# Optimization experiments

Measured on AMD Instinct MI355X. Metric: run time of the kernel, lower is better.

Reference implementation:

```python
import jax, jax.numpy as jnp
import numpy as np

L_LAYERS = 2
SEQ = 2048
K_EIG = 24
D = 128
D_TGT = 64
K_U = 3
K_Y = 2
B = 8


def hankel_eigh(n, k):
    # Z[i,j] = 2 / ((i+j)^3 - (i+j)), 1-indexed; top-k eigenpairs
    s = np.arange(1, n + 1, dtype=np.float64)
    ij = s[:, None] + s[None, :]
    z = 2.0 / (ij ** 3 - ij)
    vals, vecs = np.linalg.eigh(z)
    return (jnp.asarray(vals[-k:], jnp.float32), jnp.asarray(vecs[:, -k:], jnp.float32))


def setup_inputs() -> dict:
    key = jax.random.key(0)
    ks = jax.random.split(key, 8)
    sd = 1.0 / np.sqrt(D)
    inp = {
        "x": jax.random.normal(ks[0], (B, SEQ, D), jnp.float32),
        "emb_w": jax.random.normal(ks[1], (D, D), jnp.float32) * sd,
        "emb_b": jnp.zeros((D,), jnp.float32),
        "ln_g": jnp.ones((L_LAYERS, D), jnp.float32),
        "ln_b": jnp.zeros((L_LAYERS, D), jnp.float32),
        "m_phi": jax.random.normal(ks[2], (L_LAYERS, K_EIG * D, D), jnp.float32) * sd,
        "m_u": jax.random.normal(ks[3], (L_LAYERS, D, D, K_U), jnp.float32) * sd,
        "m_y": jax.random.normal(ks[4], (L_LAYERS, D, K_Y, D), jnp.float32) * 0.01,
        "w1": jax.random.normal(ks[5], (L_LAYERS, D, 2 * D), jnp.float32) * sd,
        "b1": jnp.zeros((L_LAYERS, 2 * D), jnp.float32),
        "proj_w": jax.random.normal(ks[6], (D, D_TGT), jnp.float32) * sd,
        "proj_b": jnp.zeros((D_TGT,), jnp.float32),
    }
    ev, evec = hankel_eigh(SEQ, K_EIG)
    inp["eig_vals"] = ev
    inp["eig_vecs"] = evec
    return inp


def compute_x_tilde(x, eig_vals, eig_vecs):
    # x: [B, L, D]; causal (truncated full) convolution of each eigvec filter
    # with each input channel via FFT. Result [B, L, K, D] -> [B, L, K*D].
    n = 2 * SEQ
    V = jnp.fft.rfft(eig_vecs, n=n, axis=0)              # [nf, K]
    U = jnp.fft.rfft(x, n=n, axis=1)                     # [B, nf, D]
    conv = jnp.fft.irfft(V[None, :, :, None] * U[:, :, None, :], n=n, axis=1)[:, :SEQ]
    conv = conv * (eig_vals ** 0.25)[None, None, :, None]
    return conv.reshape(x.shape[0], SEQ, K_EIG * x.shape[-1]).astype(x.dtype)


def compute_ar_x_preds(m_u, x):
    # o[t] = sum_{i<K_U} m_u[:, :, i] @ x[t-i]  (zero for t-i < 0)
    res = jnp.einsum('bli,oi->blo', x, m_u[:, :, 0])
    for i in range(1, K_U):
        xi = jnp.pad(x, ((0, 0), (i, 0), (0, 0)))[:, :SEQ]
        res = res + jnp.einsum('bli,oi->blo', xi, m_u[:, :, i])
    return res


def compute_y_t(m_y, deltas):
    # y[t] = sum_{j<K_Y} m_y[:, j, :] @ y[t-1-j] + deltas[t]
    d = deltas.shape[-1]
    def step(carry, x):  # carry [B, K_Y, d] holds y[t-1], y[t-2], ...
        out = jnp.einsum('okd,bkd->bo', m_y, carry) + x
        carry = jnp.concatenate([out[:, None, :], carry[:, :-1]], axis=1)
        return carry, out
    init = jnp.zeros((deltas.shape[0], K_Y, d), deltas.dtype)
    _, ys = jax.lax.scan(step, init, jnp.swapaxes(deltas, 0, 1))
    return jnp.swapaxes(ys, 0, 1)


def layer_norm(x, g, b):
    mu = x.mean(-1, keepdims=True)
    var = ((x - mu) ** 2).mean(-1, keepdims=True)
    return (x - mu) / jnp.sqrt(var + 1e-5) * g + b


def reference(x, emb_w, emb_b, ln_g, ln_b, m_phi, m_u, m_y, w1, b1, proj_w, proj_b, eig_vals, eig_vecs):
    h = x @ emb_w + emb_b
    for i in range(L_LAYERS):
        z = h
        h = layer_norm(h, ln_g[i], ln_b[i])
        x_tilde = compute_x_tilde(h, eig_vals, eig_vecs)       # [B, L, K*D]
        delta = x_tilde @ m_phi[i] + compute_ar_x_preds(m_u[i], h)
        y = compute_y_t(m_y[i], delta)
        y = jax.nn.gelu(y, approximate=False)
        y = y @ w1[i] + b1[i]
        a, g = jnp.split(y, 2, axis=-1)
        h = a * jax.nn.sigmoid(g) + z                          # GLU + residual (dropout=0)
    return h @ proj_w + proj_b
```

## Files before the change

### kernel.cpp

```cpp
#include <hip/hip_runtime.h>

typedef unsigned short u16;
typedef unsigned int u32;
typedef __bf16 bf16x8 __attribute__((ext_vector_type(8)));
typedef float f32x4 __attribute__((ext_vector_type(4)));
typedef float f32x2 __attribute__((ext_vector_type(2)));
typedef u16 u16x4 __attribute__((ext_vector_type(4)));
typedef u16 u16x8 __attribute__((ext_vector_type(8)));

#define DEV static __device__ __forceinline__

static constexpr int ROWS = 8 * 2048;
static constexpr int TAPS = 24;
static constexpr int PADR = 64;
static constexpr int DROWS = 2048 + PADR;

DEV u16 f2bf(float x) {
  u32 u = __float_as_uint(x);
  u += 0x7fffu + ((u >> 16) & 1u);
  return (u16)(u >> 16);
}

DEV void gld_lds16(const u16* g, u16* l) {
  __builtin_amdgcn_global_load_lds(
      (const __attribute__((address_space(1))) u32*)g,
      (__attribute__((address_space(3))) u32*)l, 16, 0, 0);
}


__global__ void prep_toeplitz(const float* __restrict__ evec,
                              const float* __restrict__ evals,
                              u16* __restrict__ T) {
  int k = blockIdx.x / 33, ti = blockIdx.x % 33;
  float sc = powf(evals[k], 0.25f);
  u16* out = T + (size_t)blockIdx.x * 4096;
  for (int e = threadIdx.x; e < 4096; e += 256) {
    int i = e >> 6, j = e & 63;
    int tau = (ti - 1) * 64 + i - j;
    float v = (tau >= 0 && tau < 2048) ? evec[tau * 24 + k] * sc : 0.f;
    out[e] = f2bf(v);
  }
}

__global__ __launch_bounds__(128) void hprep_kernel(const float* __restrict__ my,
                                                    u16* __restrict__ Hp) {
  const int l = blockIdx.x >> 7, j = blockIdx.x & 127;
  const int o = threadIdx.x;
  const float* M = my + (size_t)l * 32768;
  u32 mp1[64], mp2[64];
  {
    const float* r1 = M + (size_t)o * 256;
    const float* r2 = r1 + 128;
#pragma unroll
    for (int q = 0; q < 64; ++q) {
      mp1[q] = (u32)f2bf(r1[2 * q]) | ((u32)f2bf(r1[2 * q + 1]) << 16);
      mp2[q] = (u32)f2bf(r2[2 * q]) | ((u32)f2bf(r2[2 * q + 1]) << 16);
    }
  }
  __shared__ float vb[3][128];
  u16* HpL = Hp + ((size_t)l * 128 + o) * (TAPS * 128) + j;
  float v0 = (o == j) ? 1.f : 0.f;
  vb[0][o] = v0;
  vb[2][o] = 0.f;
  HpL[0] = f2bf(v0);
  __syncthreads();
  for (int tau = 1; tau < TAPS; ++tau) {
    const int a = (tau + 2) % 3;
    const int b = (tau + 1) % 3;
    const int c = tau % 3;
    const float* v1 = vb[a];
    const float* v2 = vb[b];
    float acc = 0.f;
#pragma unroll
    for (int q = 0; q < 64; ++q) {
      u32 w1 = mp1[q], w2 = mp2[q];
      float m1lo = __uint_as_float(w1 << 16);
      float m1hi = __uint_as_float(w1 & 0xffff0000u);
      float m2lo = __uint_as_float(w2 << 16);
      float m2hi = __uint_as_float(w2 & 0xffff0000u);
      acc += m1lo * v1[2 * q] + m1hi * v1[2 * q + 1];
      acc += m2lo * v2[2 * q] + m2hi * v2[2 * q + 1];
    }
    vb[c][o] = acc;
    HpL[tau * 128] = f2bf(acc);
    __syncthreads();
  }
}

__global__ __launch_bounds__(256) void prep_misc(
    const float* __restrict__ emb_w, const float* __restrict__ w1,
    const float* __restrict__ proj_w, const float* __restrict__ mphi,
    const float* __restrict__ mu, const float* __restrict__ x,
    u16* __restrict__ embT, u16* __restrict__ w1T, u16* __restrict__ projT,
    u16* __restrict__ mphiT, u16* __restrict__ xbf, u16* __restrict__ dpad,
    u16* __restrict__ xtc) {
  const int blk = blockIdx.x, tid = threadIdx.x;
  if (blk < 64) {
    int idx = blk * 256 + tid;
    int n = idx >> 7, k = idx & 127;
    embT[idx] = f2bf(emb_w[k * 128 + n]);
  } else if (blk < 320) {
    int l = (blk - 64) >> 7;
    int idx = ((blk - 64) & 127) * 256 + tid;
    int n = idx >> 7, k = idx & 127;
    w1T[l * 32768 + idx] = f2bf(w1[l * 32768 + k * 256 + n]);
  } else if (blk < 352) {
    int idx = (blk - 320) * 256 + tid;
    int n = idx >> 7, k = idx & 127;
    projT[idx] = f2bf(proj_w[k * 64 + n]);
  } else if (blk < 3808) {
    int l = (blk - 352) / 1728;
    int idx = ((blk - 352) % 1728) * 256 + tid;
    int o = idx / 3456, c = idx % 3456;
    float v;
    if (c < 3072) {
      v = mphi[(size_t)l * 3072 * 128 + (size_t)c * 128 + o];
    } else {
      int cc = c - 3072;
      int j = cc >> 7, i = cc & 127;
      v = mu[(size_t)l * 128 * 128 * 3 + ((size_t)o * 128 + i) * 3 + j];
    }
    mphiT[(size_t)l * 128 * 3456 + idx] = f2bf(v);
  } else if (blk < 5856) {
    int i = (blk - 3808) * 256 + tid;
    f32x4 v = *(const f32x4*)(x + (size_t)i * 4);
    u16x4 o;
    o[0] = f2bf(v[0]); o[1] = f2bf(v[1]); o[2] = f2bf(v[2]); o[3] = f2bf(v[3]);
    *(u16x4*)(xbf + (size_t)i * 4) = o;
  } else if (blk < 5888) {
    int i = (blk - 5856) * 256 + tid;
    int b = i >> 10, off = i & 1023;
    *(u16x8*)(dpad + (size_t)b * DROWS * 128 + off * 8) =
        (u16x8){0, 0, 0, 0, 0, 0, 0, 0};
  } else {
    for (int e = tid; e < 3072; e += 256) {
      int b = e / 384, r = e % 384;
      size_t addr;
      if (r < 256) addr = ((size_t)b * 2048 + 0) * 3456 + 3200 + r;
      else addr = ((size_t)b * 2048 + 1) * 3456 + 3328 + (r - 256);
      xtc[addr] = 0;
    }
  }
}


__global__ __launch_bounds__(256) void ln_tr_kernel(
    const float* __restrict__ h, const float* __restrict__ gam,
    const float* __restrict__ bet, u16* __restrict__ hlnT,
    u16* __restrict__ xtc) {
  __shared__ u16 tile[64][136];
  const int b = blockIdx.x >> 5, st = blockIdx.x & 31;
  const int wrow = threadIdx.x >> 6;
  const int lane = threadIdx.x & 63;
  f32x2 g2 = *(const f32x2*)(gam + lane * 2);
  f32x2 b2 = *(const f32x2*)(bet + lane * 2);
#pragma unroll 4
  for (int it = 0; it < 16; ++it) {
    int lr = it * 4 + wrow;
    int t = st * 64 + lr;
    size_t row = (size_t)b * 2048 + t;
    f32x2 v = *(const f32x2*)(h + row * 128 + lane * 2);
    float s = v[0] + v[1];
#pragma unroll
    for (int o = 32; o; o >>= 1) s += __shfl_xor(s, o);
    float mu = s * (1.f / 128.f);
    float dx = v[0] - mu, dy = v[1] - mu;
    float q = dx * dx + dy * dy;
#pragma unroll
    for (int o = 32; o; o >>= 1) q += __shfl_xor(q, o);
    float rstd = rsqrtf(q * (1.f / 128.f) + 1e-5f);
    float o0 = dx * rstd * g2[0] + b2[0];
    float o1 = dy * rstd * g2[1] + b2[1];
    u32 pk = (u32)f2bf(o0) | ((u32)f2bf(o1) << 16);
    *(u32*)&tile[lr][lane * 2] = pk;
    *(u32*)&xtc[row * 3456 + 3072 + lane * 2] = pk;
    if (t + 1 < 2048) *(u32*)&xtc[(row + 1) * 3456 + 3200 + lane * 2] = pk;
    if (t + 2 < 2048) *(u32*)&xtc[(row + 2) * 3456 + 3328 + lane * 2] = pk;
  }
  __syncthreads();
  const int d = threadIdx.x >> 1;
  const int half = threadIdx.x & 1;
#pragma unroll
  for (int i = 0; i < 4; ++i) {
    int sg = half * 4 + i;
    u16x8 w;
#pragma unroll
    for (int j = 0; j < 8; ++j) w[j] = tile[sg * 8 + j][d];
    *(u16x8*)(hlnT + ((size_t)b * 128 + d) * 2048 + st * 64 + sg * 8) = w;
  }
}


template <int BM, int BN, int WROWS, int WCOLS>
__global__ __launch_bounds__(256) void gemm_bt(
    const u16* __restrict__ A, int lda, const u16* __restrict__ BT, int ldbt,
    float* __restrict__ C, int ldc, const float* __restrict__ bias, int kBlocks) {
  constexpr int WTM = BM / WROWS;
  constexpr int WTN = BN / WCOLS;
  constexpr int FM = WTM / 16;
  constexpr int FN = WTN / 16;
  static_assert(FM >= 1 && FN >= 1, "tile too small");
  __shared__ u16 As[BM * 64];
  __shared__ u16 Bs[BN * 64];
  const int tid = threadIdx.x;
  const int wid = tid >> 6, lane = tid & 63;
  const int bm = blockIdx.x, bn = blockIdx.y;
  const int wr = wid / WCOLS, wc = wid % WCOLS;
  const int r = lane & 15, hi = lane >> 4;

  f32x4 acc[FM][FN];
#pragma unroll
  for (int i = 0; i < FM; ++i)
#pragma unroll
    for (int j = 0; j < FN; ++j) acc[i][j] = (f32x4){0.f, 0.f, 0.f, 0.f};

  for (int kb = 0; kb < kBlocks; ++kb) {
    if (kb) __syncthreads();
#pragma unroll
    for (int it = 0; it < BM / 32; ++it) {
      int ci = it * 256 + tid;
      int sc = (ci & 7) ^ ((ci >> 3) & 7);
      gld_lds16(A + (size_t)(bm * BM + (ci >> 3)) * lda + kb * 64 + sc * 8,
                &As[(it * 256 + wid * 64) * 8]);
    }
#pragma unroll
    for (int it = 0; it < BN / 32; ++it) {
      int ci = it * 256 + tid;
      int sc = (ci & 7) ^ ((ci >> 3) & 7);
      gld_lds16(BT + (size_t)(bn * BN + (ci >> 3)) * ldbt + kb * 64 + sc * 8,
                &Bs[(it * 256 + wid * 64) * 8]);
    }
    __syncthreads();
#pragma unroll
    for (int ks = 0; ks < 2; ++ks) {
      const int sk = ((ks * 4 + hi) ^ (r & 7)) << 3;
      bf16x8 af[FM], bfv[FN];
#pragma unroll
      for (int fm = 0; fm < FM; ++fm)
        af[fm] = *(const bf16x8*)&As[(wr * WTM + fm * 16 + r) * 64 + sk];
#pragma unroll
      for (int fn = 0; fn < FN; ++fn)
        bfv[fn] = *(const bf16x8*)&Bs[(wc * WTN + fn * 16 + r) * 64 + sk];
#pragma unroll
      for (int fm = 0; fm < FM; ++fm)
#pragma unroll
        for (int fn = 0; fn < FN; ++fn)
          acc[fm][fn] = __builtin_amdgcn_mfma_f32_16x16x32_bf16(
              af[fm], bfv[fn], acc[fm][fn], 0, 0, 0);
    }
  }
#pragma unroll
  for (int fm = 0; fm < FM; ++fm) {
#pragma unroll
    for (int fn = 0; fn < FN; ++fn) {
      const int col = bn * BN + wc * WTN + fn * 16 + r;
      const float bv = bias ? bias[col] : 0.f;
#pragma unroll
      for (int q = 0; q < 4; ++q) {
        const int row = bm * BM + wr * WTM + fm * 16 + hi * 4 + q;
        C[(size_t)row * ldc + col] = acc[fm][fn][q] + bv;
      }
    }
  }
}

__global__ __launch_bounds__(256) void gemm_delta(
    const u16* __restrict__ A, const u16* __restrict__ BT,
    u16* __restrict__ dpad) {
  __shared__ u16 As[2][32 * 64];
  __shared__ u16 Bs[2][128 * 64];
  const int tid = threadIdx.x;
  const int wid = tid >> 6, lane = tid & 63;
  const int bm = blockIdx.x;
  const int wr = wid >> 1, wc = wid & 1;
  const int r = lane & 15, hi = lane >> 4;

  f32x4 acc[4];
#pragma unroll
  for (int j = 0; j < 4; ++j) acc[j] = (f32x4){0.f, 0.f, 0.f, 0.f};

  auto stage = [&](int kb, int p) {
    {
      int ci = tid;
      int sc = (ci & 7) ^ ((ci >> 3) & 7);
      gld_lds16(A + (size_t)(bm * 32 + (ci >> 3)) * 3456 + kb * 64 + sc * 8,
                &As[p][(wid * 64) * 8]);
    }
#pragma unroll
    for (int it = 0; it < 4; ++it) {
      int ci = it * 256 + tid;
      int sc = (ci & 7) ^ ((ci >> 3) & 7);
      gld_lds16(BT + (size_t)(ci >> 3) * 3456 + kb * 64 + sc * 8,
                &Bs[p][(it * 256 + wid * 64) * 8]);
    }
  };

  stage(0, 0);
  __syncthreads();
  for (int kb = 0; kb < 54; ++kb) {
    const int p = kb & 1;
    if (kb < 53) stage(kb + 1, p ^ 1);
#pragma unroll
    for (int ks = 0; ks < 2; ++ks) {
      const int sk = ((ks * 4 + hi) ^ (r & 7)) << 3;
      bf16x8 af = *(const bf16x8*)&As[p][(wr * 16 + r) * 64 + sk];
      bf16x8 bfv[4];
#pragma unroll
      for (int fn = 0; fn < 4; ++fn)
        bfv[fn] = *(const bf16x8*)&Bs[p][(wc * 64 + fn * 16 + r) * 64 + sk];
#pragma unroll
      for (int fn = 0; fn < 4; ++fn)
        acc[fn] = __builtin_amdgcn_mfma_f32_16x16x32_bf16(af, bfv[fn], acc[fn], 0, 0, 0);
    }
    __syncthreads();
  }
#pragma unroll
  for (int fn = 0; fn < 4; ++fn) {
    const int col = wc * 64 + fn * 16 + r;
#pragma unroll
    for (int q = 0; q < 4; ++q) {
      const int row = bm * 32 + wr * 16 + hi * 4 + q;
      int bb = row >> 11, t = row & 2047;
      dpad[((size_t)(bb * DROWS + PADR + t)) * 128 + col] = f2bf(acc[fn][q]);
    }
  }
}

__global__ __launch_bounds__(256) void gemm_conv(
    const u16* __restrict__ T, const u16* __restrict__ hlnT,
    u16* __restrict__ xtc) {
  __shared__ u16 As[2][64 * 64];
  __shared__ u16 Bs[128 * 64];
  const int tid = threadIdx.x;
  const int wid = tid >> 6, lane = tid & 63;
  const int xcd = blockIdx.x & 7;
  const int slot = blockIdx.x >> 3;
  const int tt = slot / 24;
  const int rem24 = slot % 24;
  const int kc = (xcd >> 1) * 6 + rem24 % 6;
  const int b = (xcd & 1) * 4 + rem24 / 6;
  const int t0 = (15 - tt) << 7;
  const int r = lane & 15, hi = lane >> 4;
  const int wr = wid >> 1, wc = wid & 1;

  f32x4 acc[4][4];
#pragma unroll
  for (int i = 0; i < 4; ++i)
#pragma unroll
    for (int j = 0; j < 4; ++j) acc[i][j] = (f32x4){0.f, 0.f, 0.f, 0.f};

  const u16* Tk = T + (size_t)kc * 33 * 4096;
  const u16* Bb = hlnT + (size_t)b * 128 * 2048;
  const int base = t0 >> 6;
  const int nsb = base + 2;

  for (int sb = 0; sb < nsb; ++sb) {
    const int dlt = base - sb;
    const int p = sb & 1;
    if (sb) __syncthreads();
#pragma unroll
    for (int it = 0; it < 2; ++it) {
      int ci = it * 256 + tid;
      int sc = (ci & 7) ^ ((ci >> 3) & 7);
      gld_lds16(Tk + (size_t)(dlt + 1) * 4096 + (ci >> 3) * 64 + sc * 8,
                &As[p][(it * 256 + wid * 64) * 8]);
    }
    if (sb == 0) {
#pragma unroll
      for (int it = 0; it < 2; ++it) {
        int ci = it * 256 + tid;
        int sc = (ci & 7) ^ ((ci >> 3) & 7);
        gld_lds16(Tk + (size_t)(dlt + 2) * 4096 + (ci >> 3) * 64 + sc * 8,
                  &As[1][(it * 256 + wid * 64) * 8]);
      }
    }
#pragma unroll
    for (int it = 0; it < 4; ++it) {
      int ci = it * 256 + tid;
      int sc = (ci & 7) ^ ((ci >> 3) & 7);
      gld_lds16(Bb + (size_t)(ci >> 3) * 2048 + sb * 64 + sc * 8,
                &Bs[(it * 256 + wid * 64) * 8]);
    }
    __syncthreads();
    const u16* Aw = As[p ^ wr];
#pragma unroll
    for (int ks = 0; ks < 2; ++ks) {
      const int sk = ((ks * 4 + hi) ^ (r & 7)) << 3;
      bf16x8 af[4], bfv[4];
#pragma unroll
      for (int fm = 0; fm < 4; ++fm)
        af[fm] = *(const bf16x8*)&Aw[(fm * 16 + r) * 64 + sk];
#pragma unroll
      for (int fn = 0; fn < 4; ++fn)
        bfv[fn] = *(const bf16x8*)&Bs[(wc * 64 + fn * 16 + r) * 64 + sk];
#pragma unroll
      for (int fm = 0; fm < 4; ++fm)
#pragma unroll
        for (int fn = 0; fn < 4; ++fn)
          acc[fm][fn] = __builtin_amdgcn_mfma_f32_16x16x32_bf16(
              af[fm], bfv[fn], acc[fm][fn], 0, 0, 0);
    }
  }
#pragma unroll
  for (int fm = 0; fm < 4; ++fm) {
#pragma unroll
    for (int fn = 0; fn < 4; ++fn) {
      const int col = wc * 64 + fn * 16 + r;
#pragma unroll
      for (int q = 0; q < 4; ++q) {
        const int row = t0 + wr * 64 + fm * 16 + hi * 4 + q;
        xtc[((size_t)(b * 2048 + row)) * 3456 + kc * 128 + col] = f2bf(acc[fm][fn][q]);
      }
    }
  }
}

__global__ __launch_bounds__(256) void gemm_yconv(
    const u16* __restrict__ dpad, const u16* __restrict__ Hp,
    u16* __restrict__ ybf) {
  __shared__ u16 As[64 * 128];
  __shared__ u16 Bs[64 * 128];
  const int tid = threadIdx.x;
  const int wid = tid >> 6, lane = tid & 63;
  const int bm = blockIdx.x, bn = blockIdx.y;
  const int b = bm >> 5, t0 = (bm & 31) << 6;
  const int r = lane & 15, hi = lane >> 4;

  f32x4 acc[4];
#pragma unroll
  for (int j = 0; j < 4; ++j) acc[j] = (f32x4){0.f, 0.f, 0.f, 0.f};

  const u16* Ab = dpad + (size_t)b * DROWS * 128;
  for (int tap = 0; tap < TAPS; ++tap) {
    const u16* Ap = Ab + (size_t)(PADR + t0 - tap) * 128;
    if (tap) __syncthreads();
#pragma unroll
    for (int it = 0; it < 4; ++it) {
      int ci = it * 256 + tid;
      int row = ci >> 4;
      int sc = (ci & 15) ^ (row & 7);
      gld_lds16(Ap + (size_t)row * 128 + sc * 8,
                &As[(it * 256 + wid * 64) * 8]);
    }
#pragma unroll
    for (int it = 0; it < 4; ++it) {
      int ci = it * 256 + tid;
      int row = ci >> 4;
      int sc = (ci & 15) ^ (row & 7);
      gld_lds16(Hp + (size_t)(bn * 64 + row) * (TAPS * 128) + tap * 128 + sc * 8,
                &Bs[(it * 256 + wid * 64) * 8]);
    }
    __syncthreads();
#pragma unroll
    for (int ks = 0; ks < 4; ++ks) {
      const int sk = ((ks * 4 + hi) ^ (r & 7)) << 3;
      bf16x8 af = *(const bf16x8*)&As[(wid * 16 + r) * 128 + sk];
      bf16x8 bfv[4];
#pragma unroll
      for (int fn = 0; fn < 4; ++fn)
        bfv[fn] = *(const bf16x8*)&Bs[(fn * 16 + r) * 128 + sk];
#pragma unroll
      for (int fn = 0; fn < 4; ++fn)
        acc[fn] = __builtin_amdgcn_mfma_f32_16x16x32_bf16(af, bfv[fn], acc[fn], 0, 0, 0);
    }
  }
#pragma unroll
  for (int fn = 0; fn < 4; ++fn) {
    const int col = bn * 64 + fn * 16 + r;
#pragma unroll
    for (int q = 0; q < 4; ++q) {
      const int row = t0 + wid * 16 + hi * 4 + q;
      float v = acc[fn][q];
      float gl = 0.5f * v * (1.f + erff(v * 0.70710678118654752f));
      ybf[((size_t)(b * 2048 + row)) * 128 + col] = f2bf(gl);
    }
  }
}

__global__ __launch_bounds__(256) void gemm_w1glu(
    const u16* __restrict__ ybf, const u16* __restrict__ w1T,
    const float* __restrict__ b1, float* __restrict__ h,
    u16* __restrict__ hbf) {
  __shared__ u16 As[32 * 64];
  __shared__ u16 Bs[256 * 64];
  __shared__ float sg[32][128];
  const int tid = threadIdx.x;
  const int wid = tid >> 6, lane = tid & 63;
  const int bm = blockIdx.x;
  const int wr = wid >> 1, wc = wid & 1;
  const int r = lane & 15, hi = lane >> 4;

  f32x4 acc[8];
#pragma unroll
  for (int j = 0; j < 8; ++j) acc[j] = (f32x4){0.f, 0.f, 0.f, 0.f};

  for (int kb = 0; kb < 2; ++kb) {
    if (kb) __syncthreads();
    {
      int ci = tid;
      int sc = (ci & 7) ^ ((ci >> 3) & 7);
      gld_lds16(ybf + (size_t)(bm * 32 + (ci >> 3)) * 128 + kb * 64 + sc * 8,
                &As[(wid * 64) * 8]);
    }
#pragma unroll
    for (int it = 0; it < 8; ++it) {
      int ci = it * 256 + tid;
      int sc = (ci & 7) ^ ((ci >> 3) & 7);
      gld_lds16(w1T + (size_t)(ci >> 3) * 128 + kb * 64 + sc * 8,
                &Bs[(it * 256 + wid * 64) * 8]);
    }
    __syncthreads();
#pragma unroll
    for (int ks = 0; ks < 2; ++ks) {
      const int sk = ((ks * 4 + hi) ^ (r & 7)) << 3;
      bf16x8 af = *(const bf16x8*)&As[(wr * 16 + r) * 64 + sk];
      bf16x8 bfv[8];
#pragma unroll
      for (int fn = 0; fn < 8; ++fn)
        bfv[fn] = *(const bf16x8*)&Bs[(wc * 128 + fn * 16 + r) * 64 + sk];
#pragma unroll
      for (int fn = 0; fn < 8; ++fn)
        acc[fn] = __builtin_amdgcn_mfma_f32_16x16x32_bf16(af, bfv[fn], acc[fn], 0, 0, 0);
    }
  }
  __syncthreads();
  if (wc == 1) {
#pragma unroll
    for (int fn = 0; fn < 8; ++fn) {
      const int colg = fn * 16 + r;
      const float bv = b1[128 + colg];
#pragma unroll
      for (int q = 0; q < 4; ++q) {
        const int rl = wr * 16 + hi * 4 + q;
        float v = acc[fn][q] + bv;
        sg[rl][colg] = 1.f / (1.f + expf(-v));
      }
    }
  }
  __syncthreads();
  if (wc == 0) {
#pragma unroll
    for (int fn = 0; fn < 8; ++fn) {
      const int col = fn * 16 + r;
      const float bv = b1[col];
#pragma unroll
      for (int q = 0; q < 4; ++q) {
        const int rl = wr * 16 + hi * 4 + q;
        const size_t row = (size_t)bm * 32 + rl;
        float a = acc[fn][q] + bv;
        float hn = a * sg[rl][col] + h[row * 128 + col];
        h[row * 128 + col] = hn;
        hbf[row * 128 + col] = f2bf(hn);
      }
    }
  }
}


extern "C" void kernel_launch(void* const* d_in, const int* in_sizes, int n_in,
                              void* d_out, int out_size, void* d_ws, size_t ws_size,
                              hipStream_t stream) {
  (void)in_sizes; (void)n_in; (void)out_size; (void)ws_size;
  const float* x = (const float*)d_in[0];
  const float* emb_w = (const float*)d_in[1];
  const float* emb_b = (const float*)d_in[2];
  const float* ln_g = (const float*)d_in[3];
  const float* ln_b = (const float*)d_in[4];
  const float* m_phi = (const float*)d_in[5];
  const float* m_u = (const float*)d_in[6];
  const float* m_y = (const float*)d_in[7];
  const float* w1 = (const float*)d_in[8];
  const float* b1 = (const float*)d_in[9];
  const float* proj_w = (const float*)d_in[10];
  const float* proj_b = (const float*)d_in[11];
  const float* evals = (const float*)d_in[12];
  const float* evec = (const float*)d_in[13];
  float* out = (float*)d_out;

  char* p = (char*)d_ws;
  auto carve = [&](size_t bytes) {
    char* r = p;
    p += (bytes + 255) & ~(size_t)255;
    return r;
  };
  u16* Tbuf = (u16*)carve((size_t)24 * 33 * 4096 * 2);
  u16* embT = (u16*)carve(128 * 128 * 2);
  u16* w1T = (u16*)carve((size_t)2 * 256 * 128 * 2);
  u16* projT = (u16*)carve(64 * 128 * 2);
  u16* mphiT = (u16*)carve((size_t)2 * 128 * 3456 * 2);
  u16* Hp = (u16*)carve((size_t)2 * 128 * TAPS * 128 * 2);
  u16* xbf = (u16*)carve((size_t)ROWS * 128 * 2);
  float* h = (float*)carve((size_t)ROWS * 128 * 4);
  u16* hbf = (u16*)carve((size_t)ROWS * 128 * 2);
  u16* hlnT = (u16*)carve((size_t)ROWS * 128 * 2);
  u16* xtc = (u16*)carve((size_t)ROWS * 3456 * 2);
  u16* dpad = (u16*)carve((size_t)8 * DROWS * 128 * 2);
  u16* ybf = (u16*)carve((size_t)ROWS * 128 * 2);

  prep_toeplitz<<<dim3(24 * 33), dim3(256), 0, stream>>>(evec, evals, Tbuf);
  hprep_kernel<<<dim3(256), dim3(128), 0, stream>>>(m_y, Hp);
  prep_misc<<<dim3(5889), dim3(256), 0, stream>>>(
      emb_w, w1, proj_w, m_phi, m_u, x, embT, w1T, projT, mphiT, xbf, dpad, xtc);

  gemm_bt<32, 128, 2, 2><<<dim3(512, 1), dim3(256), 0, stream>>>(
      xbf, 128, embT, 128, h, 128, emb_b, 2);

  for (int l = 0; l < 2; ++l) {
    const u16* mT = mphiT + (size_t)l * 128 * 3456;
    ln_tr_kernel<<<dim3(256), dim3(256), 0, stream>>>(
        h, ln_g + l * 128, ln_b + l * 128, hlnT, xtc);
    gemm_conv<<<dim3(3072), dim3(256), 0, stream>>>(Tbuf, hlnT, xtc);
    gemm_delta<<<dim3(512), dim3(256), 0, stream>>>(xtc, mT, dpad);
    gemm_yconv<<<dim3(256, 2), dim3(256), 0, stream>>>(
        dpad, Hp + (size_t)l * 128 * TAPS * 128, ybf);
    gemm_w1glu<<<dim3(512), dim3(256), 0, stream>>>(
        ybf, w1T + (size_t)l * 256 * 128, b1 + l * 256, h, hbf);
  }

  gemm_bt<32, 64, 2, 2><<<dim3(512, 1), dim3(256), 0, stream>>>(
      hbf, 128, projT, 128, out, 64, proj_b, 2);
}
```

Before: 466.4 us.

## Double waves per block in conv/delta GEMMs and fold Toeplitz prep into prep_misc

```diff
diff --git a/kernel.cpp b/kernel.cpp
--- a/kernel.cpp
+++ b/kernel.cpp
@@ -27,20 +27,6 @@
       (__attribute__((address_space(3))) u32*)l, 16, 0, 0);
 }
 
-
-__global__ void prep_toeplitz(const float* __restrict__ evec,
-                              const float* __restrict__ evals,
-                              u16* __restrict__ T) {
-  int k = blockIdx.x / 33, ti = blockIdx.x % 33;
-  float sc = powf(evals[k], 0.25f);
-  u16* out = T + (size_t)blockIdx.x * 4096;
-  for (int e = threadIdx.x; e < 4096; e += 256) {
-    int i = e >> 6, j = e & 63;
-    int tau = (ti - 1) * 64 + i - j;
-    float v = (tau >= 0 && tau < 2048) ? evec[tau * 24 + k] * sc : 0.f;
-    out[e] = f2bf(v);
-  }
-}
 
 __global__ __launch_bounds__(128) void hprep_kernel(const float* __restrict__ my,
                                                     u16* __restrict__ Hp) {
@@ -91,9 +77,10 @@
     const float* __restrict__ emb_w, const float* __restrict__ w1,
     const float* __restrict__ proj_w, const float* __restrict__ mphi,
     const float* __restrict__ mu, const float* __restrict__ x,
+    const float* __restrict__ evec, const float* __restrict__ evals,
     u16* __restrict__ embT, u16* __restrict__ w1T, u16* __restrict__ projT,
     u16* __restrict__ mphiT, u16* __restrict__ xbf, u16* __restrict__ dpad,
-    u16* __restrict__ xtc) {
+    u16* __restrict__ xtc, u16* __restrict__ Tbuf) {
   const int blk = blockIdx.x, tid = threadIdx.x;
   if (blk < 64) {
     int idx = blk * 256 + tid;
@@ -132,13 +119,24 @@
     int b = i >> 10, off = i & 1023;
     *(u16x8*)(dpad + (size_t)b * DROWS * 128 + off * 8) =
         (u16x8){0, 0, 0, 0, 0, 0, 0, 0};
-  } else {
+  } else if (blk == 5888) {
     for (int e = tid; e < 3072; e += 256) {
       int b = e / 384, r = e % 384;
       size_t addr;
       if (r < 256) addr = ((size_t)b * 2048 + 0) * 3456 + 3200 + r;
       else addr = ((size_t)b * 2048 + 1) * 3456 + 3328 + (r - 256);
       xtc[addr] = 0;
+    }
+  } else {
+    int tb = blk - 5889;
+    int k = tb / 33, ti = tb % 33;
+    float sc = powf(evals[k], 0.25f);
+    u16* outp = Tbuf + (size_t)tb * 4096;
+    for (int e = tid; e < 4096; e += 256) {
+      int i = e >> 6, j = e & 63;
+      int tau = (ti - 1) * 64 + i - j;
+      float v = (tau >= 0 && tau < 2048) ? evec[tau * 24 + k] * sc : 0.f;
+      outp[e] = f2bf(v);
     }
   }
 }
@@ -264,7 +262,7 @@
   }
 }
 
-__global__ __launch_bounds__(256) void gemm_delta(
+__global__ __launch_bounds__(512) void gemm_delta(
     const u16* __restrict__ A, const u16* __restrict__ BT,
     u16* __restrict__ dpad) {
   __shared__ u16 As[2][32 * 64];
@@ -272,26 +270,26 @@
   const int tid = threadIdx.x;
   const int wid = tid >> 6, lane = tid & 63;
   const int bm = blockIdx.x;
-  const int wr = wid >> 1, wc = wid & 1;
+  const int wr = wid >> 2, wc = wid & 3;
   const int r = lane & 15, hi = lane >> 4;
 
-  f32x4 acc[4];
-#pragma unroll
-  for (int j = 0; j < 4; ++j) acc[j] = (f32x4){0.f, 0.f, 0.f, 0.f};
+  f32x4 acc[2];
+#pragma unroll
+  for (int j = 0; j < 2; ++j) acc[j] = (f32x4){0.f, 0.f, 0.f, 0.f};
 
   auto stage = [&](int kb, int p) {
-    {
+    if (tid < 256) {
       int ci = tid;
       int sc = (ci & 7) ^ ((ci >> 3) & 7);
       gld_lds16(A + (size_t)(bm * 32 + (ci >> 3)) * 3456 + kb * 64 + sc * 8,
                 &As[p][(wid * 64) * 8]);
     }
 #pragma unroll
-    for (int it = 0; it < 4; ++it) {
-      int ci = it * 256 + tid;
+    for (int it = 0; it < 2; ++it) {
+      int ci = it * 512 + tid;
       int sc = (ci & 7) ^ ((ci >> 3) & 7);
       gld_lds16(BT + (size_t)(ci >> 3) * 3456 + kb * 64 + sc * 8,
-                &Bs[p][(it * 256 + wid * 64) * 8]);
+                &Bs[p][(it * 512 + wid * 64) * 8]);
     }
   };
 
@@ -304,19 +302,19 @@
     for (int ks = 0; ks < 2; ++ks) {
       const int sk = ((ks * 4 + hi) ^ (r & 7)) << 3;
       bf16x8 af = *(const bf16x8*)&As[p][(wr * 16 + r) * 64 + sk];
-      bf16x8 bfv[4];
-#pragma unroll
-      for (int fn = 0; fn < 4; ++fn)
-        bfv[fn] = *(const bf16x8*)&Bs[p][(wc * 64 + fn * 16 + r) * 64 + sk];
-#pragma unroll
-      for (int fn = 0; fn < 4; ++fn)
+      bf16x8 bfv[2];
+#pragma unroll
+      for (int fn = 0; fn < 2; ++fn)
+        bfv[fn] = *(const bf16x8*)&Bs[p][(wc * 32 + fn * 16 + r) * 64 + sk];
+#pragma unroll
+      for (int fn = 0; fn < 2; ++fn)
         acc[fn] = __builtin_amdgcn_mfma_f32_16x16x32_bf16(af, bfv[fn], acc[fn], 0, 0, 0);
     }
     __syncthreads();
   }
 #pragma unroll
-  for (int fn = 0; fn < 4; ++fn) {
-    const int col = wc * 64 + fn * 16 + r;
+  for (int fn = 0; fn < 2; ++fn) {
+    const int col = wc * 32 + fn * 16 + r;
 #pragma unroll
     for (int q = 0; q < 4; ++q) {
       const int row = bm * 32 + wr * 16 + hi * 4 + q;
@@ -326,7 +324,7 @@
   }
 }
 
-__global__ __launch_bounds__(256) void gemm_conv(
+__global__ __launch_bounds__(512) void gemm_conv(
     const u16* __restrict__ T, const u16* __restrict__ hlnT,
     u16* __restrict__ xtc) {
   __shared__ u16 As[2][64 * 64];
@@ -341,62 +339,54 @@
   const int b = (xcd & 1) * 4 + rem24 / 6;
   const int t0 = (15 - tt) << 7;
   const int r = lane & 15, hi = lane >> 4;
-  const int wr = wid >> 1, wc = wid & 1;
-
-  f32x4 acc[4][4];
+  const int wr = wid >> 2, wc = wid & 3;
+
+  f32x4 acc[4][2];
 #pragma unroll
   for (int i = 0; i < 4; ++i)
 #pragma unroll
-    for (int j = 0; j < 4; ++j) acc[i][j] = (f32x4){0.f, 0.f, 0.f, 0.f};
+    for (int j = 0; j < 2; ++j) acc[i][j] = (f32x4){0.f, 0.f, 0.f, 0.f};
 
   const u16* Tk = T + (size_t)kc * 33 * 4096;
   const u16* Bb = hlnT + (size_t)b * 128 * 2048;
   const int base = t0 >> 6;
   const int nsb = base + 2;
 
+  auto stageA = [&](int ti, int p) {
+    int sc = (tid & 7) ^ ((tid >> 3) & 7);
+    gld_lds16(Tk + (size_t)ti * 4096 + (tid >> 3) * 64 + sc * 8,
+              &As[p][(wid * 64) * 8]);
+  };
+
   for (int sb = 0; sb < nsb; ++sb) {
     const int dlt = base - sb;
     const int p = sb & 1;
     if (sb) __syncthreads();
+    stageA(dlt + 1, p);
+    if (sb == 0) stageA(dlt + 2, 1);
 #pragma unroll
     for (int it = 0; it < 2; ++it) {
-      int ci = it * 256 + tid;
-      int sc = (ci & 7) ^ ((ci >> 3) & 7);
-      gld_lds16(Tk + (size_t)(dlt + 1) * 4096 + (ci >> 3) * 64 + sc * 8,
-                &As[p][(it * 256 + wid * 64) * 8]);
-    }
-    if (sb == 0) {
-#pragma unroll
-      for (int it = 0; it < 2; ++it) {
-        int ci = it * 256 + tid;
-        int sc = (ci & 7) ^ ((ci >> 3) & 7);
-        gld_lds16(Tk + (size_t)(dlt + 2) * 4096 + (ci >> 3) * 64 + sc * 8,
-                  &As[1][(it * 256 + wid * 64) * 8]);
-      }
-    }
-#pragma unroll
-    for (int it = 0; it < 4; ++it) {
-      int ci = it * 256 + tid;
+      int ci = it * 512 + tid;
       int sc = (ci & 7) ^ ((ci >> 3) & 7);
       gld_lds16(Bb + (size_t)(ci >> 3) * 2048 + sb * 64 + sc * 8,
-                &Bs[(it * 256 + wid * 64) * 8]);
+                &Bs[(it * 512 + wid * 64) * 8]);
     }
     __syncthreads();
     const u16* Aw = As[p ^ wr];
 #pragma unroll
     for (int ks = 0; ks < 2; ++ks) {
       const int sk = ((ks * 4 + hi) ^ (r & 7)) << 3;
-      bf16x8 af[4], bfv[4];
+      bf16x8 af[4], bfv[2];
 #pragma unroll
       for (int fm = 0; fm < 4; ++fm)
         af[fm] = *(const bf16x8*)&Aw[(fm * 16 + r) * 64 + sk];
 #pragma unroll
-      for (int fn = 0; fn < 4; ++fn)
-        bfv[fn] = *(const bf16x8*)&Bs[(wc * 64 + fn * 16 + r) * 64 + sk];
+      for (int fn = 0; fn < 2; ++fn)
+        bfv[fn] = *(const bf16x8*)&Bs[(wc * 32 + fn * 16 + r) * 64 + sk];
 #pragma unroll
       for (int fm = 0; fm < 4; ++fm)
 #pragma unroll
-        for (int fn = 0; fn < 4; ++fn)
+        for (int fn = 0; fn < 2; ++fn)
           acc[fm][fn] = __builtin_amdgcn_mfma_f32_16x16x32_bf16(
               af[fm], bfv[fn], acc[fm][fn], 0, 0, 0);
     }
@@ -404,8 +394,8 @@
 #pragma unroll
   for (int fm = 0; fm < 4; ++fm) {
 #pragma unroll
-    for (int fn = 0; fn < 4; ++fn) {
-      const int col = wc * 64 + fn * 16 + r;
+    for (int fn = 0; fn < 2; ++fn) {
+      const int col = wc * 32 + fn * 16 + r;
 #pragma unroll
       for (int q = 0; q < 4; ++q) {
         const int row = t0 + wr * 64 + fm * 16 + hi * 4 + q;
@@ -597,10 +587,10 @@
   u16* dpad = (u16*)carve((size_t)8 * DROWS * 128 * 2);
   u16* ybf = (u16*)carve((size_t)ROWS * 128 * 2);
 
-  prep_toeplitz<<<dim3(24 * 33), dim3(256), 0, stream>>>(evec, evals, Tbuf);
   hprep_kernel<<<dim3(256), dim3(128), 0, stream>>>(m_y, Hp);
-  prep_misc<<<dim3(5889), dim3(256), 0, stream>>>(
-      emb_w, w1, proj_w, m_phi, m_u, x, embT, w1T, projT, mphiT, xbf, dpad, xtc);
+  prep_misc<<<dim3(6681), dim3(256), 0, stream>>>(
+      emb_w, w1, proj_w, m_phi, m_u, x, evec, evals,
+      embT, w1T, projT, mphiT, xbf, dpad, xtc, Tbuf);
 
   gemm_bt<32, 128, 2, 2><<<dim3(512, 1), dim3(256), 0, stream>>>(
       xbf, 128, embT, 128, h, 128, emb_b, 2);
@@ -609,8 +599,8 @@
     const u16* mT = mphiT + (size_t)l * 128 * 3456;
     ln_tr_kernel<<<dim3(256), dim3(256), 0, stream>>>(
         h, ln_g + l * 128, ln_b + l * 128, hlnT, xtc);
-    gemm_conv<<<dim3(3072), dim3(256), 0, stream>>>(Tbuf, hlnT, xtc);
-    gemm_delta<<<dim3(512), dim3(256), 0, stream>>>(xtc, mT, dpad);
+    gemm_conv<<<dim3(3072), dim3(512), 0, stream>>>(Tbuf, hlnT, xtc);
+    gemm_delta<<<dim3(512), dim3(512), 0, stream>>>(xtc, mT, dpad);
     gemm_yconv<<<dim3(256, 2), dim3(256), 0, stream>>>(
         dpad, Hp + (size_t)l * 128 * TAPS * 128, ybf);
     gemm_w1glu<<<dim3(512), dim3(256), 0, stream>>>(
```

Result: slower. 484.4 us (+3.9%).
